# Performance work log

Measured on AMD Instinct MI355X. Metric: run time of the kernel, lower is better.

## Reference

```python
import jax, jax.numpy as jnp
import numpy as np

EMB = 1024
HEADS = 16
B, N = 2, 2048

def setup_inputs() -> dict:
    key = jax.random.key(0)
    ks = jax.random.split(key, 9)
    s = 1.0 / np.sqrt(EMB)
    return {
        "x": jax.random.normal(ks[0], (B, N, EMB), dtype=jnp.float32),
        "Wq": jax.random.normal(ks[1], (EMB, EMB), dtype=jnp.float32) * s,
        "bq": jax.random.normal(ks[2], (EMB,), dtype=jnp.float32) * 0.01,
        "Wk": jax.random.normal(ks[3], (EMB, EMB), dtype=jnp.float32) * s,
        "bk": jax.random.normal(ks[4], (EMB,), dtype=jnp.float32) * 0.01,
        "Wv": jax.random.normal(ks[5], (EMB, EMB), dtype=jnp.float32) * s,
        "bv": jax.random.normal(ks[6], (EMB,), dtype=jnp.float32) * 0.01,
        "Wo": jax.random.normal(ks[7], (EMB, EMB), dtype=jnp.float32) * s,
        "bo": jax.random.normal(ks[8], (EMB,), dtype=jnp.float32) * 0.01,
    }

def _split_heads(t):
    b, n, e = t.shape
    return t.reshape(b, n, HEADS, e // HEADS).transpose(0, 2, 1, 3)  # b h n d

def reference(x, Wq, bq, Wk, bk, Wv, bv, Wo, bo):
    q = _split_heads(x @ Wq + bq)
    k = _split_heads(x @ Wk + bk)
    v = _split_heads(x @ Wv + bv)
    # NOTE: original scales by sqrt(emb_size), not sqrt(head_dim)
    scaling = jnp.asarray(EMB, x.dtype) ** 0.5
    energy = jnp.einsum('bhqd,bhkd->bhqk', q, k)
    att = jax.nn.softmax(energy / scaling, axis=-1)
    out = jnp.einsum('bhqk,bhkd->bhqd', att, v)
    out = out.transpose(0, 2, 1, 3).reshape(x.shape[0], x.shape[1], EMB)
    return out @ Wo + bo
```

## Files before the change

### kernel.cpp

```cpp
#include <hip/hip_runtime.h>
#include <hip/hip_bf16.h>

typedef __bf16 bf16_t;
typedef bf16_t bf16x8 __attribute__((ext_vector_type(8)));
typedef float f32x4 __attribute__((ext_vector_type(4)));
typedef float f32x16 __attribute__((ext_vector_type(16)));

#define EMB 1024
#define HEADS 16
#define BATCH 2
#define SEQ 2048
#define HD 64
#define TOKENS (BATCH * SEQ)

__device__ __forceinline__ void gld16(bf16_t* lds_dst, const bf16_t* g_src) {
    __builtin_amdgcn_global_load_lds(
        (const __attribute__((address_space(1))) unsigned int*)g_src,
        (__attribute__((address_space(3))) unsigned int*)lds_dst, 16, 0, 0);
}

__device__ __forceinline__ unsigned cvt_pk_bf16(float lo, float hi) {
    unsigned r;
    asm("v_cvt_pk_bf16_f32 %0, %1, %2" : "=v"(r) : "v"(lo), "v"(hi));
    return r;
}

__global__ __launch_bounds__(256) void convert_x(const float* __restrict__ x,
                                                 bf16_t* __restrict__ xb) {
    size_t i = ((size_t)blockIdx.x * 256 + threadIdx.x) * 16;
    f32x4 v0 = *(const f32x4*)&x[i];
    f32x4 v1 = *(const f32x4*)&x[i + 4];
    f32x4 v2 = *(const f32x4*)&x[i + 8];
    f32x4 v3 = *(const f32x4*)&x[i + 12];
    bf16x8 o0, o1;
#pragma unroll
    for (int j = 0; j < 4; ++j) {
        o0[j] = (bf16_t)v0[j]; o0[4 + j] = (bf16_t)v1[j];
        o1[j] = (bf16_t)v2[j]; o1[4 + j] = (bf16_t)v3[j];
    }
    *(bf16x8*)&xb[i] = o0;
    *(bf16x8*)&xb[i + 8] = o1;
}

__global__ __launch_bounds__(256) void prep_w(
    const float* __restrict__ W0, const float* __restrict__ W1,
    const float* __restrict__ W2, const float* __restrict__ W3,
    bf16_t* __restrict__ T0, bf16_t* __restrict__ T1,
    bf16_t* __restrict__ T2, bf16_t* __restrict__ T3) {
    __shared__ __align__(16) bf16_t T[64][72];
    int z = blockIdx.z;
    const float* src = (z == 0) ? W0 : (z == 1) ? W1 : (z == 2) ? W2 : W3;
    bf16_t* dst = (z == 0) ? T0 : (z == 1) ? T1 : (z == 2) ? T2 : T3;
    int k0 = blockIdx.y * 64, n0 = blockIdx.x * 64;
    int r = threadIdx.x >> 2, c4 = (threadIdx.x & 3) * 16;
    f32x4 v[4];
#pragma unroll
    for (int q = 0; q < 4; ++q)
        v[q] = *(const f32x4*)&src[(size_t)(k0 + r) * 1024 + n0 + c4 + q * 4];
#pragma unroll
    for (int j = 0; j < 16; ++j) T[c4 + j][r] = (bf16_t)v[j >> 2][j & 3];
    __syncthreads();
    bf16x8 o0 = *(const bf16x8*)&T[r][c4];
    bf16x8 o1 = *(const bf16x8*)&T[r][c4 + 8];
    *(bf16x8*)&dst[(size_t)(n0 + r) * 1024 + k0 + c4] = o0;
    *(bf16x8*)&dst[(size_t)(n0 + r) * 1024 + k0 + c4 + 8] = o1;
}

template <typename TO>
__global__ __launch_bounds__(256) void gemm128(
    const bf16_t* __restrict__ A,
    const bf16_t* __restrict__ Wt0, const bf16_t* __restrict__ Wt1, const bf16_t* __restrict__ Wt2,
    const float* __restrict__ b0, const float* __restrict__ b1, const float* __restrict__ b2,
    TO* __restrict__ o0, TO* __restrict__ o1, TO* __restrict__ o2,
    int md0, int md1, int md2, float sc0, float sc1, float sc2) {
    __shared__ __align__(16) bf16_t As[128 * 32];
    __shared__ __align__(16) bf16_t Bs[128 * 32];

    const int tid = threadIdx.x, w = tid >> 6, lane = tid & 63;
    const int quad = lane >> 4, c = lane & 15;
    const int wm = (w >> 1) * 64, wn = (w & 1) * 64;
    const int m0 = blockIdx.y * 128, n0 = blockIdx.x * 128;

    const int z = blockIdx.z;
    const bf16_t* W = (z == 0) ? Wt0 : (z == 1) ? Wt1 : Wt2;
    const float* bias = (z == 0) ? b0 : (z == 1) ? b1 : b2;
    TO* out = (z == 0) ? o0 : (z == 1) ? o1 : o2;
    const int mode = (z == 0) ? md0 : (z == 1) ? md1 : md2;
    const float scale = (z == 0) ? sc0 : (z == 1) ? sc1 : sc2;

    f32x4 acc[4][4];
#pragma unroll
    for (int i = 0; i < 4; ++i)
#pragma unroll
        for (int j = 0; j < 4; ++j) acc[i][j] = (f32x4){0.f, 0.f, 0.f, 0.f};

    const int srow = lane >> 2, schunk = lane & 3;
    const bf16_t* Ag = A + (size_t)m0 * 1024;
    const bf16_t* Bg = W + (size_t)n0 * 1024;

    for (int k0 = 0; k0 < 1024; k0 += 32) {
        __syncthreads();
#pragma unroll
        for (int s = 0; s < 2; ++s) {
            int rg = (w * 2 + s) * 16;
            gld16(&As[rg * 32], &Ag[(size_t)(rg + srow) * 1024 + k0 + schunk * 8]);
            gld16(&Bs[rg * 32], &Bg[(size_t)(rg + srow) * 1024 + k0 + schunk * 8]);
        }
        __syncthreads();

        bf16x8 af[4], bfv[4];
#pragma unroll
        for (int t = 0; t < 4; ++t)
            af[t] = *(const bf16x8*)&As[(wm + t * 16 + c) * 32 + quad * 8];
#pragma unroll
        for (int t = 0; t < 4; ++t)
            bfv[t] = *(const bf16x8*)&Bs[(wn + t * 16 + c) * 32 + quad * 8];
#pragma unroll
        for (int mt = 0; mt < 4; ++mt)
#pragma unroll
            for (int nt = 0; nt < 4; ++nt)
                acc[mt][nt] = __builtin_amdgcn_mfma_f32_16x16x32_bf16(
                    af[mt], bfv[nt], acc[mt][nt], 0, 0, 0);
    }

#pragma unroll
    for (int nt = 0; nt < 4; ++nt) {
        int col = n0 + wn + nt * 16 + c;
        float bv = bias[col];
#pragma unroll
        for (int mt = 0; mt < 4; ++mt)
#pragma unroll
            for (int r = 0; r < 4; ++r) {
                int row = m0 + wm + mt * 16 + quad * 4 + r;
                float v = (acc[mt][nt][r] + bv) * scale;
                size_t idx;
                if (mode == 0) {
                    idx = (size_t)row * 1024 + col;
                } else {
                    int bb = row >> 11, n = row & 2047;
                    int hh = col >> 6, d = col & 63;
                    idx = (mode == 1) ? ((size_t)(bb * HEADS + hh) * SEQ + n) * HD + d
                                      : ((size_t)(bb * HEADS + hh) * HD + d) * SEQ + n;
                }
                out[idx] = (TO)v;
            }
    }
}

__global__ __launch_bounds__(256) void attn_kernel(
    const bf16_t* __restrict__ Q, const bf16_t* __restrict__ K,
    const bf16_t* __restrict__ Vt, bf16_t* __restrict__ O) {
    __shared__ __align__(16) bf16_t Qs[128 * 64];
    __shared__ __align__(16) bf16_t Ks[2][64 * 64];
    __shared__ __align__(16) bf16_t Vs[2][64 * 64];

    const int tid = threadIdx.x, w = tid >> 6, lane = tid & 63;
    const int hi = lane >> 5, lq = lane & 31;
    const int bh = blockIdx.y, b = bh >> 4, h = bh & 15;
    const int q0 = blockIdx.x * 128;

    const int srow8 = lane >> 3, sch = lane & 7;

    const bf16_t* Qg = Q + ((size_t)bh * SEQ + q0) * HD;
    const bf16_t* Kg0 = K + (size_t)bh * SEQ * HD;
    const bf16_t* Vg0 = Vt + (size_t)bh * HD * SEQ;

#pragma unroll
    for (int s = 0; s < 4; ++s) {
        int rg = (w * 4 + s) * 8;
        int row = rg + srow8;
        int g = sch ^ (row & 7);
        gld16(&Qs[rg * 64], &Qg[(size_t)row * 64 + g * 8]);
    }
#pragma unroll
    for (int s = 0; s < 2; ++s) {
        int rg = (w * 2 + s) * 8;
        int row = rg + srow8;
        int g = sch ^ (row & 7);
        gld16(&Ks[0][rg * 64], &Kg0[(size_t)row * 64 + g * 8]);
        gld16(&Vs[0][rg * 64], &Vg0[(size_t)row * SEQ + g * 8]);
    }
    __syncthreads();

    bf16x8 qf[4];
    {
        int row = w * 32 + lq;
#pragma unroll
        for (int dc = 0; dc < 4; ++dc)
            qf[dc] = *(const bf16x8*)&Qs[row * 64 + (((dc * 2 + hi) ^ (row & 7)) * 8)];
    }

    f32x16 Oacc0, Oacc1;
#pragma unroll
    for (int r = 0; r < 16; ++r) { Oacc0[r] = 0.f; Oacc1[r] = 0.f; }
    float lp = 0.f;

    for (int t = 0; t < SEQ / 64; ++t) {
        const int cur = t & 1;
        if (t + 1 < SEQ / 64) {
            const bf16_t* Kg = Kg0 + (size_t)(t + 1) * 64 * HD;
            const bf16_t* Vg = Vg0 + (t + 1) * 64;
#pragma unroll
            for (int s = 0; s < 2; ++s) {
                int rg = (w * 2 + s) * 8;
                int row = rg + srow8;
                int g = sch ^ (row & 7);
                gld16(&Ks[cur ^ 1][rg * 64], &Kg[(size_t)row * 64 + g * 8]);
                gld16(&Vs[cur ^ 1][rg * 64], &Vg[(size_t)row * SEQ + g * 8]);
            }
        }

        f32x16 St0, St1;
#pragma unroll
        for (int r = 0; r < 16; ++r) { St0[r] = 0.f; St1[r] = 0.f; }
        __builtin_amdgcn_s_setprio(1);
#pragma unroll
        for (int dc = 0; dc < 4; ++dc) {
            int r0 = lq, r1 = 32 + lq;
            bf16x8 k0 = *(const bf16x8*)&Ks[cur][r0 * 64 + (((dc * 2 + hi) ^ (r0 & 7)) * 8)];
            bf16x8 k1 = *(const bf16x8*)&Ks[cur][r1 * 64 + (((dc * 2 + hi) ^ (r1 & 7)) * 8)];
            St0 = __builtin_amdgcn_mfma_f32_32x32x16_bf16(k0, qf[dc], St0, 0, 0, 0);
            St1 = __builtin_amdgcn_mfma_f32_32x32x16_bf16(k1, qf[dc], St1, 0, 0, 0);
        }
        __builtin_amdgcn_s_setprio(0);

#pragma unroll
        for (int r = 0; r < 16; ++r) {
            St0[r] = __expf(St0[r]); lp += St0[r];
            St1[r] = __expf(St1[r]); lp += St1[r];
        }

        bf16x8 pf[4];
#define PACKFRAG(SS, c2, dstIdx)                                              \
        {                                                                      \
            unsigned pa = cvt_pk_bf16(SS[8 * (c2) + 0], SS[8 * (c2) + 1]);     \
            unsigned pb = cvt_pk_bf16(SS[8 * (c2) + 4], SS[8 * (c2) + 5]);     \
            unsigned pc = cvt_pk_bf16(SS[8 * (c2) + 2], SS[8 * (c2) + 3]);     \
            unsigned pd = cvt_pk_bf16(SS[8 * (c2) + 6], SS[8 * (c2) + 7]);     \
            asm volatile("v_permlane32_swap_b32 %0, %1" : "+v"(pa), "+v"(pb)); \
            asm volatile("v_permlane32_swap_b32 %0, %1" : "+v"(pc), "+v"(pd)); \
            union { unsigned u[4]; bf16x8 v; } pu;                             \
            pu.u[0] = pa; pu.u[1] = pc; pu.u[2] = pb; pu.u[3] = pd;            \
            pf[dstIdx] = pu.v;                                                 \
        }
        PACKFRAG(St0, 0, 0)
        PACKFRAG(St0, 1, 1)
        PACKFRAG(St1, 0, 2)
        PACKFRAG(St1, 1, 3)
#undef PACKFRAG

        __builtin_amdgcn_s_setprio(1);
#pragma unroll
        for (int f = 0; f < 4; ++f) {
            int d0 = lq, d1 = 32 + lq;
            bf16x8 v0 = *(const bf16x8*)&Vs[cur][d0 * 64 + (((f * 2 + hi) ^ (d0 & 7)) * 8)];
            bf16x8 v1 = *(const bf16x8*)&Vs[cur][d1 * 64 + (((f * 2 + hi) ^ (d1 & 7)) * 8)];
            Oacc0 = __builtin_amdgcn_mfma_f32_32x32x16_bf16(pf[f], v0, Oacc0, 0, 0, 0);
            Oacc1 = __builtin_amdgcn_mfma_f32_32x32x16_bf16(pf[f], v1, Oacc1, 0, 0, 0);
        }
        __builtin_amdgcn_s_setprio(0);

        __syncthreads();
    }

    lp += __shfl_xor(lp, 32);
    float rl = 1.0f / lp;

#pragma unroll
    for (int r = 0; r < 16; ++r) {
        int q_loc = (r & 3) + 8 * (r >> 2) + 4 * hi;
        float rr = __shfl(rl, q_loc);
        int qrow = q0 + w * 32 + q_loc;
        size_t base = ((size_t)(b * SEQ + qrow)) * EMB + h * 64;
        O[base + lq] = (bf16_t)(Oacc0[r] * rr);
        O[base + 32 + lq] = (bf16_t)(Oacc1[r] * rr);
    }
}

extern "C" void kernel_launch(void* const* d_in, const int* in_sizes, int n_in,
                              void* d_out, int out_size, void* d_ws, size_t ws_size,
                              hipStream_t stream) {
    (void)in_sizes; (void)n_in; (void)out_size; (void)ws_size;
    const float* x  = (const float*)d_in[0];
    const float* Wq = (const float*)d_in[1];
    const float* bq = (const float*)d_in[2];
    const float* Wk = (const float*)d_in[3];
    const float* bk = (const float*)d_in[4];
    const float* Wv = (const float*)d_in[5];
    const float* bv = (const float*)d_in[6];
    const float* Wo = (const float*)d_in[7];
    const float* bo = (const float*)d_in[8];

    bf16_t* ws = (bf16_t*)d_ws;
    const size_t NELEM = (size_t)TOKENS * EMB;
    const size_t WELEM = (size_t)EMB * EMB;
    bf16_t* Qb  = ws;
    bf16_t* Kb  = ws + NELEM;
    bf16_t* Vb  = ws + 2 * NELEM;
    bf16_t* Ob  = ws + 3 * NELEM;
    bf16_t* xb  = ws + 4 * NELEM;
    bf16_t* Wt0 = ws + 5 * NELEM;
    bf16_t* Wt1 = Wt0 + WELEM;
    bf16_t* Wt2 = Wt0 + 2 * WELEM;
    bf16_t* Wt3 = Wt0 + 3 * WELEM;

    hipLaunchKernelGGL(convert_x, dim3(1024), dim3(256), 0, stream, x, xb);
    hipLaunchKernelGGL(prep_w, dim3(16, 16, 4), dim3(256), 0, stream,
                       Wq, Wk, Wv, Wo, Wt0, Wt1, Wt2, Wt3);
    hipLaunchKernelGGL((gemm128<bf16_t>), dim3(8, 32, 3), dim3(256), 0, stream,
                       xb, Wt0, Wt1, Wt2, bq, bk, bv, Qb, Kb, Vb,
                       1, 1, 2, 0.03125f, 1.0f, 1.0f);
    hipLaunchKernelGGL(attn_kernel, dim3(16, 32), dim3(256), 0, stream, Qb, Kb, Vb, Ob);
    hipLaunchKernelGGL((gemm128<float>), dim3(8, 32, 1), dim3(256), 0, stream,
                       Ob, Wt3, Wt3, Wt3, bo, bo, bo,
                       (float*)d_out, (float*)d_out, (float*)d_out,
                       0, 0, 0, 1.0f, 1.0f, 1.0f);
}
```

Baseline: 209.7 us.

## Add separate V transpose kernel, exp2 softmax, XCD-aware attention block mapping

The V projection now writes the same coalesced head-major layout as Q and K, and a new small kernel transposes V into the d-major layout that attention reads. The strided scattered stores in the QKV GEMM epilogue go away at the cost of one extra launch and an extra read and write of V. The Q scale is folded with log2(e) so softmax can use the hardware exp2. Attention blocks are remapped so that blocks sharing a head land on the same XCD, and the KV loop is unrolled by two with precomputed LDS and global offsets.

```diff
diff --git a/kernel.cpp b/kernel.cpp
--- a/kernel.cpp
+++ b/kernel.cpp
@@ -23,6 +23,14 @@
     unsigned r;
     asm("v_cvt_pk_bf16_f32 %0, %1, %2" : "=v"(r) : "v"(lo), "v"(hi));
     return r;
+}
+
+__device__ __forceinline__ float exp2_fast(float x) {
+#if __has_builtin(__builtin_amdgcn_exp2f)
+    return __builtin_amdgcn_exp2f(x);
+#else
+    return __expf(x * 0.69314718056f);
+#endif
 }
 
 __global__ __launch_bounds__(256) void convert_x(const float* __restrict__ x,
@@ -66,6 +74,24 @@
     *(bf16x8*)&dst[(size_t)(n0 + r) * 1024 + k0 + c4 + 8] = o1;
 }
 
+__global__ __launch_bounds__(256) void vtrans(const bf16_t* __restrict__ V,
+                                              bf16_t* __restrict__ Vt) {
+    __shared__ __align__(16) bf16_t T[64][72];
+    int bh = blockIdx.y, n0 = blockIdx.x * 64;
+    int r = threadIdx.x >> 2, c4 = (threadIdx.x & 3) * 16;
+    const bf16_t* src = &V[((size_t)bh * SEQ + n0 + r) * HD + c4];
+    bf16x8 v0 = *(const bf16x8*)&src[0];
+    bf16x8 v1 = *(const bf16x8*)&src[8];
+#pragma unroll
+    for (int j = 0; j < 8; ++j) { T[c4 + j][r] = v0[j]; T[c4 + 8 + j][r] = v1[j]; }
+    __syncthreads();
+    bf16x8 o0 = *(const bf16x8*)&T[r][c4];
+    bf16x8 o1 = *(const bf16x8*)&T[r][c4 + 8];
+    bf16_t* dst = &Vt[((size_t)bh * HD + r) * SEQ + n0 + c4];
+    *(bf16x8*)&dst[0] = o0;
+    *(bf16x8*)&dst[8] = o1;
+}
+
 template <typename TO>
 __global__ __launch_bounds__(256) void gemm128(
     const bf16_t* __restrict__ A,
@@ -139,8 +165,7 @@
                 } else {
                     int bb = row >> 11, n = row & 2047;
                     int hh = col >> 6, d = col & 63;
-                    idx = (mode == 1) ? ((size_t)(bb * HEADS + hh) * SEQ + n) * HD + d
-                                      : ((size_t)(bb * HEADS + hh) * HD + d) * SEQ + n;
+                    idx = ((size_t)(bb * HEADS + hh) * SEQ + n) * HD + d;
                 }
                 out[idx] = (TO)v;
             }
@@ -156,14 +181,33 @@
 
     const int tid = threadIdx.x, w = tid >> 6, lane = tid & 63;
     const int hi = lane >> 5, lq = lane & 31;
-    const int bh = blockIdx.y, b = bh >> 4, h = bh & 15;
-    const int q0 = blockIdx.x * 128;
+
+    const int lin = blockIdx.x + (blockIdx.y << 4);
+    const int xcd = lin & 7, slot = lin >> 3;
+    const int bh = xcd + ((slot >> 4) << 3);
+    const int q0 = (slot & 15) << 7;
+    const int b = bh >> 4, h = bh & 15;
 
     const int srow8 = lane >> 3, sch = lane & 7;
 
     const bf16_t* Qg = Q + ((size_t)bh * SEQ + q0) * HD;
     const bf16_t* Kg0 = K + (size_t)bh * SEQ * HD;
     const bf16_t* Vg0 = Vt + (size_t)bh * HD * SEQ;
+
+    int sl[2], sgK[2], sgV[2];
+#pragma unroll
+    for (int s = 0; s < 2; ++s) {
+        int rg = (w * 2 + s) * 8;
+        int row = rg + srow8;
+        int g = sch ^ (row & 7);
+        sl[s] = rg * 64;
+        sgK[s] = row * 64 + g * 8;
+        sgV[s] = row * SEQ + g * 8;
+    }
+    int rd[4];
+#pragma unroll
+    for (int dc = 0; dc < 4; ++dc)
+        rd[dc] = lq * 64 + (((dc * 2 + hi) ^ (lq & 7)) * 8);
 
 #pragma unroll
     for (int s = 0; s < 4; ++s) {
@@ -174,64 +218,67 @@
     }
 #pragma unroll
     for (int s = 0; s < 2; ++s) {
-        int rg = (w * 2 + s) * 8;
-        int row = rg + srow8;
-        int g = sch ^ (row & 7);
-        gld16(&Ks[0][rg * 64], &Kg0[(size_t)row * 64 + g * 8]);
-        gld16(&Vs[0][rg * 64], &Vg0[(size_t)row * SEQ + g * 8]);
+        gld16(&Ks[0][sl[s]], &Kg0[sgK[s]]);
+        gld16(&Vs[0][sl[s]], &Vg0[sgV[s]]);
     }
     __syncthreads();
 
     bf16x8 qf[4];
-    {
-        int row = w * 32 + lq;
-#pragma unroll
-        for (int dc = 0; dc < 4; ++dc)
-            qf[dc] = *(const bf16x8*)&Qs[row * 64 + (((dc * 2 + hi) ^ (row & 7)) * 8)];
-    }
+#pragma unroll
+    for (int dc = 0; dc < 4; ++dc)
+        qf[dc] = *(const bf16x8*)&Qs[w * 2048 + rd[dc]];
 
     f32x16 Oacc0, Oacc1;
 #pragma unroll
     for (int r = 0; r < 16; ++r) { Oacc0[r] = 0.f; Oacc1[r] = 0.f; }
     float lp = 0.f;
 
-    for (int t = 0; t < SEQ / 64; ++t) {
-        const int cur = t & 1;
-        if (t + 1 < SEQ / 64) {
-            const bf16_t* Kg = Kg0 + (size_t)(t + 1) * 64 * HD;
-            const bf16_t* Vg = Vg0 + (t + 1) * 64;
-#pragma unroll
-            for (int s = 0; s < 2; ++s) {
-                int rg = (w * 2 + s) * 8;
-                int row = rg + srow8;
-                int g = sch ^ (row & 7);
-                gld16(&Ks[cur ^ 1][rg * 64], &Kg[(size_t)row * 64 + g * 8]);
-                gld16(&Vs[cur ^ 1][rg * 64], &Vg[(size_t)row * SEQ + g * 8]);
-            }
-        }
-
-        f32x16 St0, St1;
-#pragma unroll
-        for (int r = 0; r < 16; ++r) { St0[r] = 0.f; St1[r] = 0.f; }
-        __builtin_amdgcn_s_setprio(1);
-#pragma unroll
-        for (int dc = 0; dc < 4; ++dc) {
-            int r0 = lq, r1 = 32 + lq;
-            bf16x8 k0 = *(const bf16x8*)&Ks[cur][r0 * 64 + (((dc * 2 + hi) ^ (r0 & 7)) * 8)];
-            bf16x8 k1 = *(const bf16x8*)&Ks[cur][r1 * 64 + (((dc * 2 + hi) ^ (r1 & 7)) * 8)];
-            St0 = __builtin_amdgcn_mfma_f32_32x32x16_bf16(k0, qf[dc], St0, 0, 0, 0);
-            St1 = __builtin_amdgcn_mfma_f32_32x32x16_bf16(k1, qf[dc], St1, 0, 0, 0);
-        }
-        __builtin_amdgcn_s_setprio(0);
-
-#pragma unroll
-        for (int r = 0; r < 16; ++r) {
-            St0[r] = __expf(St0[r]); lp += St0[r];
-            St1[r] = __expf(St1[r]); lp += St1[r];
-        }
-
-        bf16x8 pf[4];
-#define PACKFRAG(SS, c2, dstIdx)                                              \
+    const bf16_t* KgN = Kg0 + 64 * HD;
+    const bf16_t* VgN = Vg0 + 64;
+
+#define ATTN_STEP(TT, CUR)                                                     \
+    {                                                                          \
+        if ((TT) + 1 < SEQ / 64) {                                             \
+            _Pragma("unroll")                                                  \
+            for (int s = 0; s < 2; ++s) {                                      \
+                gld16(&Ks[(CUR) ^ 1][sl[s]], &KgN[sgK[s]]);                    \
+                gld16(&Vs[(CUR) ^ 1][sl[s]], &VgN[sgV[s]]);                    \
+            }                                                                  \
+            KgN += 64 * HD; VgN += 64;                                         \
+        }                                                                      \
+        f32x16 St0, St1;                                                       \
+        _Pragma("unroll")                                                      \
+        for (int r = 0; r < 16; ++r) { St0[r] = 0.f; St1[r] = 0.f; }           \
+        __builtin_amdgcn_s_setprio(1);                                         \
+        _Pragma("unroll")                                                      \
+        for (int dc = 0; dc < 4; ++dc) {                                       \
+            bf16x8 k0 = *(const bf16x8*)&Ks[CUR][rd[dc]];                      \
+            bf16x8 k1 = *(const bf16x8*)&Ks[CUR][rd[dc] + 2048];               \
+            St0 = __builtin_amdgcn_mfma_f32_32x32x16_bf16(k0, qf[dc], St0, 0, 0, 0); \
+            St1 = __builtin_amdgcn_mfma_f32_32x32x16_bf16(k1, qf[dc], St1, 0, 0, 0); \
+        }                                                                      \
+        __builtin_amdgcn_s_setprio(0);                                         \
+        _Pragma("unroll")                                                      \
+        for (int r = 0; r < 16; ++r) {                                         \
+            St0[r] = exp2_fast(St0[r]); lp += St0[r];                          \
+            St1[r] = exp2_fast(St1[r]); lp += St1[r];                          \
+        }                                                                      \
+        bf16x8 pf[4];                                                          \
+        PACKFRAG(St0, 0, 0) PACKFRAG(St0, 1, 1)                                \
+        PACKFRAG(St1, 0, 2) PACKFRAG(St1, 1, 3)                                \
+        __builtin_amdgcn_s_setprio(1);                                         \
+        _Pragma("unroll")                                                      \
+        for (int f = 0; f < 4; ++f) {                                          \
+            bf16x8 v0 = *(const bf16x8*)&Vs[CUR][rd[f]];                       \
+            bf16x8 v1 = *(const bf16x8*)&Vs[CUR][rd[f] + 2048];                \
+            Oacc0 = __builtin_amdgcn_mfma_f32_32x32x16_bf16(pf[f], v0, Oacc0, 0, 0, 0); \
+            Oacc1 = __builtin_amdgcn_mfma_f32_32x32x16_bf16(pf[f], v1, Oacc1, 0, 0, 0); \
+        }                                                                      \
+        __builtin_amdgcn_s_setprio(0);                                         \
+        __syncthreads();                                                       \
+    }
+
+#define PACKFRAG(SS, c2, dstIdx)                                               \
         {                                                                      \
             unsigned pa = cvt_pk_bf16(SS[8 * (c2) + 0], SS[8 * (c2) + 1]);     \
             unsigned pb = cvt_pk_bf16(SS[8 * (c2) + 4], SS[8 * (c2) + 5]);     \
@@ -243,25 +290,13 @@
             pu.u[0] = pa; pu.u[1] = pc; pu.u[2] = pb; pu.u[3] = pd;            \
             pf[dstIdx] = pu.v;                                                 \
         }
-        PACKFRAG(St0, 0, 0)
-        PACKFRAG(St0, 1, 1)
-        PACKFRAG(St1, 0, 2)
-        PACKFRAG(St1, 1, 3)
+
+    for (int t = 0; t < SEQ / 64; t += 2) {
+        ATTN_STEP(t, 0)
+        ATTN_STEP(t + 1, 1)
+    }
+#undef ATTN_STEP
 #undef PACKFRAG
-
-        __builtin_amdgcn_s_setprio(1);
-#pragma unroll
-        for (int f = 0; f < 4; ++f) {
-            int d0 = lq, d1 = 32 + lq;
-            bf16x8 v0 = *(const bf16x8*)&Vs[cur][d0 * 64 + (((f * 2 + hi) ^ (d0 & 7)) * 8)];
-            bf16x8 v1 = *(const bf16x8*)&Vs[cur][d1 * 64 + (((f * 2 + hi) ^ (d1 & 7)) * 8)];
-            Oacc0 = __builtin_amdgcn_mfma_f32_32x32x16_bf16(pf[f], v0, Oacc0, 0, 0, 0);
-            Oacc1 = __builtin_amdgcn_mfma_f32_32x32x16_bf16(pf[f], v1, Oacc1, 0, 0, 0);
-        }
-        __builtin_amdgcn_s_setprio(0);
-
-        __syncthreads();
-    }
 
     lp += __shfl_xor(lp, 32);
     float rl = 1.0f / lp;
@@ -299,6 +334,7 @@
     bf16_t* Vb  = ws + 2 * NELEM;
     bf16_t* Ob  = ws + 3 * NELEM;
     bf16_t* xb  = ws + 4 * NELEM;
+    bf16_t* Vtb = xb;
     bf16_t* Wt0 = ws + 5 * NELEM;
     bf16_t* Wt1 = Wt0 + WELEM;
     bf16_t* Wt2 = Wt0 + 2 * WELEM;
@@ -309,8 +345,9 @@
                        Wq, Wk, Wv, Wo, Wt0, Wt1, Wt2, Wt3);
     hipLaunchKernelGGL((gemm128<bf16_t>), dim3(8, 32, 3), dim3(256), 0, stream,
                        xb, Wt0, Wt1, Wt2, bq, bk, bv, Qb, Kb, Vb,
-                       1, 1, 2, 0.03125f, 1.0f, 1.0f);
-    hipLaunchKernelGGL(attn_kernel, dim3(16, 32), dim3(256), 0, stream, Qb, Kb, Vb, Ob);
+                       1, 1, 1, 0.0450842204f, 1.0f, 1.0f);
+    hipLaunchKernelGGL(vtrans, dim3(32, 32), dim3(256), 0, stream, Vb, Vtb);
+    hipLaunchKernelGGL(attn_kernel, dim3(16, 32), dim3(256), 0, stream, Qb, Kb, Vtb, Ob);
     hipLaunchKernelGGL((gemm128<float>), dim3(8, 32, 1), dim3(256), 0, stream,
                        Ob, Wt3, Wt3, Wt3, bo, bo, bo,
                        (float*)d_out, (float*)d_out, (float*)d_out,
```

Result: slower. 214.9 us (+2.5%).
